# Kernel optimization log

Hardware: AMD Instinct MI355X
Metric: run time of the kernel (lower is better)

## Reference

```python
import jax, jax.numpy as jnp
import numpy as np

N = 10000
E = 160000
HEADS = 4
HC = 32      # hidden_channels
OC = 64      # out_channels
NG = 16      # n_goods
H1, H2 = 512, 256
NEG_SLOPE = 0.2


def setup_inputs() -> dict:
    key = jax.random.key(0)
    ks = jax.random.split(key, 32)
    rn = lambda k, s, sc=0.05: (jax.random.normal(k, s, jnp.float32) * sc)
    inp = {
        "x": jax.random.normal(ks[0], (N, 63), jnp.float32),
        "next_demand": jax.random.normal(ks[1], (N, 1), jnp.float32),
        "edge_index": jax.random.randint(ks[2], (2, E), 0, N),
        "eps": jax.random.normal(ks[3], (E, NG), jnp.float32),
        "Wl3": rn(ks[4], (HEADS * HC, 64)), "Wr3": rn(ks[5], (HEADS * HC, 64)),
        "att3": rn(ks[6], (HEADS, HC)), "b3": rn(ks[7], (HEADS * HC,)),
        # gat4: 128 -> 64, 1 head, mean
        "Wl4": rn(ks[8], (OC, HEADS * HC)), "Wr4": rn(ks[9], (OC, HEADS * HC)),
        "att4": rn(ks[10], (1, OC)), "b4": rn(ks[11], (OC,)),
        "Wl1": rn(ks[12], (HEADS * HC, OC)), "Wr1": rn(ks[13], (HEADS * HC, OC)),
        "att1": rn(ks[14], (HEADS, HC)), "b1": rn(ks[15], (HEADS * HC,)),
        # gat2: 128 -> 64, 1 head, mean
        "Wl2": rn(ks[16], (OC, HEADS * HC)), "Wr2": rn(ks[17], (OC, HEADS * HC)),
        "att2": rn(ks[18], (1, OC)), "b2": rn(ks[19], (OC,)),
        # MLP head: 256 -> 512 -> 256 -> n_goods (mu, std)
        "W_fc": rn(ks[20], (H1, OC * 4)), "b_fc": rn(ks[21], (H1,)),
        "W_fc1": rn(ks[22], (H2, H1)), "b_fc1": rn(ks[23], (H2,)),
        "W_mu": rn(ks[24], (NG, H2)), "b_mu": rn(ks[25], (NG,)),
        "W_std": rn(ks[26], (NG, H2)), "b_std": rn(ks[27], (NG,)),
    }
    return inp


def gatv2(x, src, dst, n, Wl, Wr, att, bias, heads, oc, concat):
    # GATv2Conv: e = a . LeakyReLU(Wl x_src + Wr x_dst), softmax over dst neighborhoods
    xl = (x @ Wl.T).reshape(n, heads, oc)
    xr = (x @ Wr.T).reshape(n, heads, oc)
    e = jax.nn.leaky_relu(xl[src] + xr[dst], NEG_SLOPE)        # [E', H, C]
    score = jnp.einsum('ehc,hc->eh', e, att)                   # [E', H]
    m = jax.ops.segment_max(score, dst, num_segments=n)        # stable segment softmax
    ex = jnp.exp(score - m[dst])
    den = jax.ops.segment_sum(ex, dst, num_segments=n)
    alpha = ex / (den[dst] + 1e-16)
    out = jax.ops.segment_sum(alpha[:, :, None] * xl[src], dst, num_segments=n)
    out = out.reshape(n, heads * oc) if concat else out.mean(axis=1)
    return out + bias


def reference(x, next_demand, edge_index, eps,
              Wl3, Wr3, att3, b3, Wl4, Wr4, att4, b4,
              Wl1, Wr1, att1, b1, Wl2, Wr2, att2, b2,
              W_fc, b_fc, W_fc1, b_fc1, W_mu, b_mu, W_std, b_std):
    n = x.shape[0]
    lrelu = lambda v: jax.nn.leaky_relu(v, NEG_SLOPE)
    loop = jnp.arange(n)
    # forward edges + self loops (PyG GATv2Conv add_self_loops=True)
    src = jnp.concatenate([edge_index[0], loop])
    dst = jnp.concatenate([edge_index[1], loop])
    # reverse edges + self loops
    rsrc = jnp.concatenate([edge_index[1], loop])
    rdst = jnp.concatenate([edge_index[0], loop])

    h = jnp.concatenate([x, next_demand.reshape(n, -1)], axis=1)   # [N, 64]
    xb = lrelu(gatv2(h, rsrc, rdst, n, Wl3, Wr3, att3, b3, HEADS, HC, True))
    xb = lrelu(gatv2(xb, rsrc, rdst, n, Wl4, Wr4, att4, b4, 1, OC, False))
    xf = lrelu(gatv2(xb, src, dst, n, Wl1, Wr1, att1, b1, HEADS, HC, True))
    xf = lrelu(gatv2(xf, src, dst, n, Wl2, Wr2, att2, b2, 1, OC, False))

    s = jnp.concatenate([xf, xb], axis=1)                          # [N, 128]
    se = jnp.concatenate([s[edge_index[0]], s[edge_index[1]]], axis=1)  # [E, 256]
    se = jax.nn.relu(se @ W_fc.T + b_fc)
    se = jax.nn.relu(se @ W_fc1.T + b_fc1)
    mu = se @ W_mu.T + b_mu
    std = jax.nn.softplus(se @ W_std.T + b_std)

    action = mu + std * eps                                        # rsample
    log2pi = jnp.log(2.0 * jnp.pi).astype(mu.dtype)
    lp = -0.5 * ((action - mu) / std) ** 2 - jnp.log(std) - 0.5 * log2pi
    log_prob = lp.reshape(1, -1).sum(-1, keepdims=True)            # num_graphs=1
    real_action = jnp.tanh(action)
    real_log_prob = log_prob - jnp.log(1.0 - real_action ** 2 + 1e-7).reshape(1, -1).sum(-1, keepdims=True)
    return (real_action.reshape(-1), real_log_prob)
```

## Files before the change

kernel.cpp:

```cpp
#include <hip/hip_runtime.h>
#include <hip/hip_bf16.h>
#include <math.h>

typedef __attribute__((ext_vector_type(8))) short short8;
typedef __attribute__((ext_vector_type(4))) float floatx4;

#define LRELU_S 0.2f
#define HALF_LOG_2PI 0.91893853320467274178f

__device__ __forceinline__ short f2bf(float f) {
  union { float f; unsigned u; } x; x.f = f;
  unsigned r = x.u + 0x7FFFu + ((x.u >> 16) & 1u);
  return (short)(r >> 16);
}
__device__ __forceinline__ float lrelu(float v) { return v > 0.f ? v : LRELU_S * v; }
__device__ __forceinline__ float frcp(float v) { return __builtin_amdgcn_rcpf(v); }
__device__ __forceinline__ float ftanh(float x) {
  float e = __expf(2.f * x);
  return 1.f - 2.f * frcp(e + 1.f);
}
__device__ __forceinline__ int swzb(int row) {
  return ((((row >> 2) & 3) << 1) | (row & 1)) << 4;
}

__global__ __launch_bounds__(256) void k_pre(const int* __restrict__ ei,
    int* __restrict__ degF, int* __restrict__ degR, int E,
    const float* __restrict__ x, const float* __restrict__ nd,
    float* __restrict__ h, int NH,
    const float* __restrict__ Wfc, const float* __restrict__ Wfc1,
    const float* __restrict__ Wmu, const float* __restrict__ Wstd,
    short* __restrict__ WBF, int nbE, int nbH) {
  int b = blockIdx.x;
  if (b < nbE) {
    int e = b * 256 + threadIdx.x;
    if (e < E) {
      int a = ei[e], bb = ei[E + e];
      atomicAdd(degF + bb, 1);
      atomicAdd(degR + a, 1);
    }
  } else if (b < nbE + nbH) {
    int t = (b - nbE) * 256 + threadIdx.x;
    if (t < NH) {
      int n = t >> 6, j = t & 63;
      h[t] = (j < 63) ? x[n * 63 + j] : nd[n];
    }
  } else {
    int t = (b - nbE - nbH) * 256 + threadIdx.x;
    if (t < 270336) {
      int tile = t >> 9, pos = t & 511;
      int lane = pos >> 3, j = pos & 7;
      int lr = lane & 15, lg = lane >> 4;
      float v;
      if (tile < 256) {
        int nt = tile >> 3, kk = tile & 7;
        v = Wfc[(nt * 16 + lr) * 256 + kk * 32 + lg * 8 + j];
      } else if (tile < 512) {
        int t2 = tile - 256;
        int nt = t2 >> 4, kk = t2 & 15;
        v = Wfc1[(nt * 16 + lr) * 512 + kk * 32 + lg * 8 + j];
      } else {
        int t3 = tile - 512;
        int nt = t3 >> 3, kk = t3 & 7;
        int r = nt * 16 + lr;
        int col = kk * 32 + lg * 8 + j;
        v = (r < 16) ? Wmu[r * 256 + col] : Wstd[(r - 16) * 256 + col];
      }
      WBF[t] = f2bf(v);
    }
  }
}

__global__ __launch_bounds__(1024) void k_scan2(const int* __restrict__ degF,
    int* __restrict__ startF, int* __restrict__ curF, int* __restrict__ csrF,
    const int* __restrict__ degR, int* __restrict__ startR, int* __restrict__ curR,
    int* __restrict__ csrR, int n) {
  const int* __restrict__ deg = blockIdx.x ? degR : degF;
  int* __restrict__ start = blockIdx.x ? startR : startF;
  int* __restrict__ cur   = blockIdx.x ? curR : curF;
  int* __restrict__ csr   = blockIdx.x ? csrR : csrF;
  __shared__ int wsum[16];
  int t = threadIdx.x;
  int chunk = (n + 1023) >> 10;
  int lo = t * chunk; if (lo > n) lo = n;
  int hi = lo + chunk; if (hi > n) hi = n;
  int s = 0;
  for (int i = lo; i < hi; i++) s += deg[i] + 1;
  int lane = t & 63, wv = t >> 6;
  int inc = s;
  #pragma unroll
  for (int o = 1; o < 64; o <<= 1) {
    int v = __shfl_up(inc, o, 64);
    if (lane >= o) inc += v;
  }
  if (lane == 63) wsum[wv] = inc;
  __syncthreads();
  if (t < 64) {
    int v = (t < 16) ? wsum[t] : 0;
    #pragma unroll
    for (int o = 1; o < 16; o <<= 1) {
      int u = __shfl_up(v, o, 64);
      if (t >= o) v += u;
    }
    if (t < 16) wsum[t] = v;
  }
  __syncthreads();
  int base = (wv ? wsum[wv - 1] : 0) + (inc - s);
  if (t == 0) start[n] = wsum[15];
  int acc = base;
  for (int i = lo; i < hi; i++) {
    start[i] = acc; cur[i] = acc;
    acc += deg[i] + 1;
    csr[acc - 1] = i;
  }
}

__global__ __launch_bounds__(256) void k_scatter(const int* __restrict__ ei,
    int* __restrict__ curF, int* __restrict__ curR,
    int* __restrict__ csrF, int* __restrict__ csrR, int E) {
  int e = blockIdx.x * 256 + threadIdx.x;
  if (e >= E) return;
  int a = ei[e], b = ei[E + e];
  int pf = atomicAdd(curF + b, 1); csrF[pf] = a;
  int pr = atomicAdd(curR + a, 1); csrR[pr] = b;
}

template<int K, int F>
__global__ __launch_bounds__(256) void k_node_gemm(const float* __restrict__ in,
    const float* __restrict__ Wl, const float* __restrict__ Wr,
    float* __restrict__ xl, float* __restrict__ xr, int n) {
  __shared__ float sx[32][K + 1];
  const int row0 = blockIdx.x * 32;
  const float* __restrict__ W = blockIdx.y ? Wr : Wl;
  float* __restrict__ out = blockIdx.y ? xr : xl;
  const int tid = threadIdx.x;
  for (int i = tid; i < 32 * K; i += 256) {
    int r = i / K, c = i - r * K;
    sx[r][c] = (row0 + r < n) ? in[(size_t)(row0 + r) * K + c] : 0.f;
  }
  __syncthreads();
  const int nl = tid & 31;
  const int fg = tid >> 5;
  const int row = row0 + nl;
  if (row >= n) return;
  constexpr int FP = F / 8;
  for (int i = 0; i < FP; i++) {
    int f = fg * FP + i;
    const float* __restrict__ wrow = W + (size_t)f * K;
    float acc = 0.f;
    #pragma unroll
    for (int k = 0; k < K; k += 4) {
      float4 wv = *(const float4*)(wrow + k);
      acc += sx[nl][k] * wv.x + sx[nl][k + 1] * wv.y
           + sx[nl][k + 2] * wv.z + sx[nl][k + 3] * wv.w;
    }
    out[(size_t)row * F + f] = acc;
  }
}

template<int HF, int C, int OM>
__global__ __launch_bounds__(256) void k_gat_fused(const float* __restrict__ XL,
    const float* __restrict__ XR, const float* __restrict__ att,
    const float* __restrict__ bias, const int* __restrict__ start,
    const int* __restrict__ csr, float* __restrict__ out,
    short* __restrict__ sout, int scol, int n) {
  constexpr int G = HF / 4;
  constexpr int DPB = 256 / G;
  int d = blockIdx.x * DPB + threadIdx.x / G;
  if (d >= n) return;
  int f4 = threadIdx.x & (G - 1);
  float4 xr = *(const float4*)(XR + (size_t)d * HF + f4 * 4);
  float4 av = *(const float4*)(att + f4 * 4);
  float4 bv = *(const float4*)(bias + f4 * 4);
  float m = -INFINITY, den = 0.f;
  float4 acc = {0.f, 0.f, 0.f, 0.f};
  int j0 = start[d], j1 = start[d + 1];

  auto score = [&](const float4& xl) {
    float e0 = xl.x + xr.x; e0 = e0 > 0.f ? e0 : LRELU_S * e0;
    float e1 = xl.y + xr.y; e1 = e1 > 0.f ? e1 : LRELU_S * e1;
    float e2 = xl.z + xr.z; e2 = e2 > 0.f ? e2 : LRELU_S * e2;
    float e3 = xl.w + xr.w; e3 = e3 > 0.f ? e3 : LRELU_S * e3;
    float p = av.x * e0 + av.y * e1 + av.z * e2 + av.w * e3;
    #pragma unroll
    for (int o = C / 8; o > 0; o >>= 1) p += __shfl_xor(p, o, 64);
    return p;
  };

  int j = j0;
  for (; j + 1 < j1; j += 2) {
    int sa = csr[j], sb = csr[j + 1];
    float4 xla = *(const float4*)(XL + (size_t)sa * HF + f4 * 4);
    float4 xlb = *(const float4*)(XL + (size_t)sb * HF + f4 * 4);
    float sca = score(xla);
    float scb = score(xlb);
    float mn = fmaxf(fmaxf(m, sca), scb);
    float scale = __expf(m - mn);
    float pa = __expf(sca - mn);
    float pb = __expf(scb - mn);
    den = den * scale + pa + pb;
    acc.x = acc.x * scale + pa * xla.x + pb * xlb.x;
    acc.y = acc.y * scale + pa * xla.y + pb * xlb.y;
    acc.z = acc.z * scale + pa * xla.z + pb * xlb.z;
    acc.w = acc.w * scale + pa * xla.w + pb * xlb.w;
    m = mn;
  }
  if (j < j1) {
    int s = csr[j];
    float4 xl = *(const float4*)(XL + (size_t)s * HF + f4 * 4);
    float sc = score(xl);
    float mn = fmaxf(m, sc);
    float scale = __expf(m - mn);
    float p = __expf(sc - mn);
    den = den * scale + p;
    acc.x = acc.x * scale + p * xl.x;
    acc.y = acc.y * scale + p * xl.y;
    acc.z = acc.z * scale + p * xl.z;
    acc.w = acc.w * scale + p * xl.w;
    m = mn;
  }
  float inv = frcp(den + 1e-16f);
  float4 o4;
  o4.x = lrelu(acc.x * inv + bv.x);
  o4.y = lrelu(acc.y * inv + bv.y);
  o4.z = lrelu(acc.z * inv + bv.z);
  o4.w = lrelu(acc.w * inv + bv.w);
  if (OM != 2) *(float4*)(out + (size_t)d * HF + f4 * 4) = o4;
  if (OM != 0) {
    union { short s[4]; int2 v; } u;
    u.s[0] = f2bf(o4.x); u.s[1] = f2bf(o4.y);
    u.s[2] = f2bf(o4.z); u.s[3] = f2bf(o4.w);
    *(int2*)(sout + (size_t)d * 128 + scol + f4 * 4) = u.v;
  }
}

__device__ __forceinline__ short8 lds_frag(const char* base, int row, int strideB, int k0, int lg) {
  int off = row * strideB + (((k0 * 2) + lg * 16) ^ swzb(row));
  return *(const short8*)(base + off);
}

__global__ __launch_bounds__(512, 4) void k_head(
    const short* __restrict__ SBF, const short* __restrict__ WBF,
    const int* __restrict__ ei, const float* __restrict__ epsg,
    const float* __restrict__ b_fc, const float* __restrict__ b_fc1,
    const float* __restrict__ b_mu, const float* __restrict__ b_std,
    float* __restrict__ out, double* __restrict__ LP, int E) {
  __shared__ __align__(16) char lX[32768];
  __shared__ __align__(16) char cbuf[16384];
  float* lMS  = (float*)cbuf;
  float* lred = (float*)(cbuf + 8192);

  const int tid = threadIdx.x;
  const int eg0 = blockIdx.x * 64;

  for (int q = tid; q < 2048; q += 512) {
    int le = q >> 5, c = q & 31;
    int eg = eg0 + le;
    int node = (c < 16) ? ei[eg] : ei[E + eg];
    const short* srcp = SBF + (size_t)node * 128 + (c & 15) * 8;
    int4 v = *(const int4*)srcp;
    int col = (c * 16) ^ swzb(le);
    *(int4*)(lX + le * 512 + col) = v;
  }
  __syncthreads();

  const int w = tid >> 6, lane = tid & 63;
  const int lr = lane & 15, lg = lane >> 4;
  const floatx4 zero = {0.f, 0.f, 0.f, 0.f};

  floatx4 acc2[2][4];
  #pragma unroll
  for (int a = 0; a < 2; a++)
    #pragma unroll
    for (int b = 0; b < 4; b++) acc2[a][b] = zero;

  for (int c = 0; c < 4; c++) {
    floatx4 acc1[4];
    #pragma unroll
    for (int mi = 0; mi < 4; mi++) acc1[mi] = zero;
    for (int kk = 0; kk < 8; kk++) {
      int tile = (c * 8 + w) * 8 + kk;
      short8 b = *(const short8*)(WBF + tile * 512 + lane * 8);
      #pragma unroll
      for (int mi = 0; mi < 4; mi++) {
        short8 a = lds_frag(lX, mi * 16 + lr, 512, kk * 32, lg);
        acc1[mi] = __builtin_amdgcn_mfma_f32_16x16x32_bf16(a, b, acc1[mi], 0, 0, 0);
      }
    }
    __syncthreads();
    {
      int cl = w * 16 + lr;
      float bv = b_fc[c * 128 + cl];
      #pragma unroll
      for (int mi = 0; mi < 4; mi++)
        #pragma unroll
        for (int j = 0; j < 4; j++) {
          int row = mi * 16 + lg * 4 + j;
          float v = acc1[mi][j] + bv;
          v = v > 0.f ? v : 0.f;
          *(short*)(cbuf + row * 256 + ((cl * 2) ^ swzb(row))) = f2bf(v);
        }
    }
    __syncthreads();

    for (int kk2 = 0; kk2 < 4; kk2++) {
      short8 a[4];
      #pragma unroll
      for (int mi = 0; mi < 4; mi++) a[mi] = lds_frag(cbuf, mi * 16 + lr, 256, kk2 * 32, lg);
      #pragma unroll
      for (int ni2 = 0; ni2 < 2; ni2++) {
        int tile = 256 + (2 * w + ni2) * 16 + (c * 4 + kk2);
        short8 b = *(const short8*)(WBF + tile * 512 + lane * 8);
        #pragma unroll
        for (int mi = 0; mi < 4; mi++)
          acc2[ni2][mi] = __builtin_amdgcn_mfma_f32_16x16x32_bf16(a[mi], b, acc2[ni2][mi], 0, 0, 0);
      }
    }
  }
  __syncthreads();

  #pragma unroll
  for (int ni2 = 0; ni2 < 2; ni2++) {
    int n = (2 * w + ni2) * 16 + lr;
    float bv = b_fc1[n];
    #pragma unroll
    for (int mi = 0; mi < 4; mi++)
      #pragma unroll
      for (int j = 0; j < 4; j++) {
        int row = mi * 16 + lg * 4 + j;
        float v = acc2[ni2][mi][j] + bv;
        v = v > 0.f ? v : 0.f;
        *(short*)(lX + row * 512 + ((n * 2) ^ swzb(row))) = f2bf(v);
      }
  }
  __syncthreads();

  {
    const int mfr = w >> 1, nfr = w & 1;
    floatx4 acc3 = zero;
    for (int kk = 0; kk < 8; kk++) {
      short8 a = lds_frag(lX, mfr * 16 + lr, 512, kk * 32, lg);
      int tile = 512 + nfr * 8 + kk;
      short8 b = *(const short8*)(WBF + tile * 512 + lane * 8);
      acc3 = __builtin_amdgcn_mfma_f32_16x16x32_bf16(a, b, acc3, 0, 0, 0);
    }
    int coln = nfr * 16 + lr;
    float bv = (coln < 16) ? b_mu[coln] : b_std[coln - 16];
    #pragma unroll
    for (int j = 0; j < 4; j++) {
      int row = mfr * 16 + lg * 4 + j;
      lMS[row * 32 + coln] = acc3[j] + bv;
    }
  }
  __syncthreads();

  float lpsum = 0.f;
  #pragma unroll
  for (int it = 0; it < 2; it++) {
    int idx = tid + it * 512;
    int m = idx >> 4, g = idx & 15;
    float mu = lMS[m * 32 + g];
    float sr = lMS[m * 32 + 16 + g];
    float sd = (sr > 20.f) ? sr : __logf(1.f + __expf(sr));
    int eg = eg0 + m;
    float ep = epsg[(size_t)eg * 16 + g];
    float action = mu + sd * ep;
    float ra = ftanh(action);
    out[(size_t)eg * 16 + g] = ra;
    lpsum += -0.5f * ep * ep - __logf(sd) - HALF_LOG_2PI - __logf(1.f - ra * ra + 1e-7f);
  }
  #pragma unroll
  for (int o = 32; o > 0; o >>= 1) lpsum += __shfl_xor(lpsum, o, 64);
  if (lane == 0) lred[w] = lpsum;
  __syncthreads();
  if (tid == 0) {
    double ssum = 0.0;
    #pragma unroll
    for (int i = 0; i < 8; i++) ssum += (double)lred[i];
    atomicAdd(LP, ssum);
  }
}

__global__ void k_finalize(const double* __restrict__ LP, float* __restrict__ out, int pos) {
  out[pos] = (float)(*LP);
}

extern "C" void kernel_launch(void* const* d_in, const int* in_sizes, int n_in,
                              void* d_out, int out_size, void* d_ws, size_t ws_size,
                              hipStream_t stream) {
  const float* x    = (const float*)d_in[0];
  const float* nd   = (const float*)d_in[1];
  const int*   ei   = (const int*)d_in[2];
  const float* epsg = (const float*)d_in[3];
  const float* Wl3 = (const float*)d_in[4];  const float* Wr3 = (const float*)d_in[5];
  const float* att3 = (const float*)d_in[6]; const float* b3 = (const float*)d_in[7];
  const float* Wl4 = (const float*)d_in[8];  const float* Wr4 = (const float*)d_in[9];
  const float* att4 = (const float*)d_in[10]; const float* b4 = (const float*)d_in[11];
  const float* Wl1 = (const float*)d_in[12]; const float* Wr1 = (const float*)d_in[13];
  const float* att1 = (const float*)d_in[14]; const float* b1 = (const float*)d_in[15];
  const float* Wl2 = (const float*)d_in[16]; const float* Wr2 = (const float*)d_in[17];
  const float* att2 = (const float*)d_in[18]; const float* b2 = (const float*)d_in[19];
  const float* W_fc  = (const float*)d_in[20]; const float* b_fc  = (const float*)d_in[21];
  const float* W_fc1 = (const float*)d_in[22]; const float* b_fc1 = (const float*)d_in[23];
  const float* W_mu  = (const float*)d_in[24]; const float* b_mu  = (const float*)d_in[25];
  const float* W_std = (const float*)d_in[26]; const float* b_std = (const float*)d_in[27];

  const int N = in_sizes[0] / 63;
  const int E = in_sizes[2] / 2;
  const int E2 = E + N;
  const size_t NN = (size_t)N;

  char* base = (char*)d_ws;
  auto alloc = [&](size_t bytes) { char* p = base; base += (bytes + 15) & ~(size_t)15; return p; };

  int* degF   = (int*)alloc(NN * 4);
  int* degR   = (int*)alloc(NN * 4);
  double* LPp = (double*)alloc(16);
  float* bufA = (float*)alloc(NN * 128 * 4);
  float* bufB = (float*)alloc(NN * 128 * 4);
  float* XL   = (float*)alloc(NN * 128 * 4);
  float* XR   = (float*)alloc(NN * 128 * 4);
  float* XBp  = (float*)alloc(NN * 64 * 4);
  int* curF   = (int*)alloc(NN * 4);
  int* curR   = (int*)alloc(NN * 4);
  int* startF = (int*)alloc((NN + 1) * 4);
  int* startR = (int*)alloc((NN + 1) * 4);
  int* csrF   = (int*)alloc((size_t)E2 * 4);
  int* csrR   = (int*)alloc((size_t)E2 * 4);
  short* SBF  = (short*)alloc(NN * 128 * 2);
  short* WBF  = (short*)alloc(270336 * 2);

  auto nb = [](int total) { return (total + 255) / 256; };
  const int nbE = nb(E), nbH = nb(N * 64), nbW = nb(270336);

  hipMemsetAsync(degF, 0, NN * 8 + 16, stream);

  k_pre<<<nbE + nbH + nbW, 256, 0, stream>>>(ei, degF, degR, E, x, nd, bufA, N * 64,
                                             W_fc, W_fc1, W_mu, W_std, WBF, nbE, nbH);
  k_scan2<<<2, 1024, 0, stream>>>(degF, startF, curF, csrF, degR, startR, curR, csrR, N);
  k_scatter<<<nbE, 256, 0, stream>>>(ei, curF, curR, csrF, csrR, E);

  { dim3 g((N + 31) / 32, 2);
    k_node_gemm<64, 128><<<g, 256, 0, stream>>>(bufA, Wl3, Wr3, XL, XR, N); }
  k_gat_fused<128, 32, 0><<<(N + 7) / 8, 256, 0, stream>>>(XL, XR, att3, b3, startR, csrR, bufB, nullptr, 0, N);

  { dim3 g((N + 31) / 32, 2);
    k_node_gemm<128, 64><<<g, 256, 0, stream>>>(bufB, Wl4, Wr4, XL, XR, N); }
  k_gat_fused<64, 64, 1><<<(N + 15) / 16, 256, 0, stream>>>(XL, XR, att4, b4, startR, csrR, XBp, SBF, 64, N);

  { dim3 g((N + 31) / 32, 2);
    k_node_gemm<64, 128><<<g, 256, 0, stream>>>(XBp, Wl1, Wr1, XL, XR, N); }
  k_gat_fused<128, 32, 0><<<(N + 7) / 8, 256, 0, stream>>>(XL, XR, att1, b1, startF, csrF, bufB, nullptr, 0, N);

  { dim3 g((N + 31) / 32, 2);
    k_node_gemm<128, 64><<<g, 256, 0, stream>>>(bufB, Wl2, Wr2, XL, XR, N); }
  k_gat_fused<64, 64, 2><<<(N + 15) / 16, 256, 0, stream>>>(XL, XR, att2, b2, startF, csrF, nullptr, SBF, 0, N);

  k_head<<<E / 64, 512, 0, stream>>>(SBF, WBF, ei, epsg, b_fc, b_fc1, b_mu, b_std,
                                     (float*)d_out, LPp, E);
  k_finalize<<<1, 1, 0, stream>>>(LPp, (float*)d_out, E * 16);
}
```

Baseline: 434.1 us.

## Fuse next-layer node projection into GAT aggregation kernels and concat into first GEMM

Each GAT aggregation kernel now keeps its per-node output in shared memory and immediately computes the next layer's left/right projections, writing them into ping-pong XL/XR buffers. This drops three separate node-GEMM launches and the round trip of intermediate activations through global memory. The x/next_demand concatenation moves from k_pre into the first node GEMM's load loop. In exchange, each aggregation block now does a small GEMM that rereads the weight rows per output and adds a block barrier, which may lower occupancy and lengthen each aggregation kernel.

```diff
diff --git a/kernel.cpp b/kernel.cpp
--- a/kernel.cpp
+++ b/kernel.cpp
@@ -25,11 +25,9 @@
 
 __global__ __launch_bounds__(256) void k_pre(const int* __restrict__ ei,
     int* __restrict__ degF, int* __restrict__ degR, int E,
-    const float* __restrict__ x, const float* __restrict__ nd,
-    float* __restrict__ h, int NH,
     const float* __restrict__ Wfc, const float* __restrict__ Wfc1,
     const float* __restrict__ Wmu, const float* __restrict__ Wstd,
-    short* __restrict__ WBF, int nbE, int nbH) {
+    short* __restrict__ WBF, int nbE) {
   int b = blockIdx.x;
   if (b < nbE) {
     int e = b * 256 + threadIdx.x;
@@ -38,14 +36,8 @@
       atomicAdd(degF + bb, 1);
       atomicAdd(degR + a, 1);
     }
-  } else if (b < nbE + nbH) {
+  } else {
     int t = (b - nbE) * 256 + threadIdx.x;
-    if (t < NH) {
-      int n = t >> 6, j = t & 63;
-      h[t] = (j < 63) ? x[n * 63 + j] : nd[n];
-    }
-  } else {
-    int t = (b - nbE - nbH) * 256 + threadIdx.x;
     if (t < 270336) {
       int tile = t >> 9, pos = t & 511;
       int lane = pos >> 3, j = pos & 7;
@@ -124,18 +116,21 @@
   int pr = atomicAdd(curR + a, 1); csrR[pr] = b;
 }
 
-template<int K, int F>
-__global__ __launch_bounds__(256) void k_node_gemm(const float* __restrict__ in,
-    const float* __restrict__ Wl, const float* __restrict__ Wr,
-    float* __restrict__ xl, float* __restrict__ xr, int n) {
+__global__ __launch_bounds__(256) void k_node_gemm0(const float* __restrict__ x,
+    const float* __restrict__ nd, const float* __restrict__ Wl,
+    const float* __restrict__ Wr, float* __restrict__ xl, float* __restrict__ xr, int n) {
+  constexpr int K = 64, F = 128;
   __shared__ float sx[32][K + 1];
   const int row0 = blockIdx.x * 32;
   const float* __restrict__ W = blockIdx.y ? Wr : Wl;
   float* __restrict__ out = blockIdx.y ? xr : xl;
   const int tid = threadIdx.x;
   for (int i = tid; i < 32 * K; i += 256) {
-    int r = i / K, c = i - r * K;
-    sx[r][c] = (row0 + r < n) ? in[(size_t)(row0 + r) * K + c] : 0.f;
+    int r = i >> 6, c = i & 63;
+    int row = row0 + r;
+    float v = 0.f;
+    if (row < n) v = (c < 63) ? x[row * 63 + c] : nd[row];
+    sx[r][c] = v;
   }
   __syncthreads();
   const int nl = tid & 31;
@@ -157,79 +152,109 @@
   }
 }
 
-template<int HF, int C, int OM>
-__global__ __launch_bounds__(256) void k_gat_fused(const float* __restrict__ XL,
+template<int HF, int C, int OUTK, int OM>
+__global__ __launch_bounds__(256) void k_gat_gemm(const float* __restrict__ XL,
     const float* __restrict__ XR, const float* __restrict__ att,
     const float* __restrict__ bias, const int* __restrict__ start,
-    const int* __restrict__ csr, float* __restrict__ out,
+    const int* __restrict__ csr,
+    const float* __restrict__ Wl, const float* __restrict__ Wr,
+    float* __restrict__ oXL, float* __restrict__ oXR,
     short* __restrict__ sout, int scol, int n) {
   constexpr int G = HF / 4;
   constexpr int DPB = 256 / G;
-  int d = blockIdx.x * DPB + threadIdx.x / G;
-  if (d >= n) return;
-  int f4 = threadIdx.x & (G - 1);
-  float4 xr = *(const float4*)(XR + (size_t)d * HF + f4 * 4);
-  float4 av = *(const float4*)(att + f4 * 4);
-  float4 bv = *(const float4*)(bias + f4 * 4);
-  float m = -INFINITY, den = 0.f;
-  float4 acc = {0.f, 0.f, 0.f, 0.f};
-  int j0 = start[d], j1 = start[d + 1];
-
-  auto score = [&](const float4& xl) {
-    float e0 = xl.x + xr.x; e0 = e0 > 0.f ? e0 : LRELU_S * e0;
-    float e1 = xl.y + xr.y; e1 = e1 > 0.f ? e1 : LRELU_S * e1;
-    float e2 = xl.z + xr.z; e2 = e2 > 0.f ? e2 : LRELU_S * e2;
-    float e3 = xl.w + xr.w; e3 = e3 > 0.f ? e3 : LRELU_S * e3;
-    float p = av.x * e0 + av.y * e1 + av.z * e2 + av.w * e3;
-    #pragma unroll
-    for (int o = C / 8; o > 0; o >>= 1) p += __shfl_xor(p, o, 64);
-    return p;
-  };
-
-  int j = j0;
-  for (; j + 1 < j1; j += 2) {
-    int sa = csr[j], sb = csr[j + 1];
-    float4 xla = *(const float4*)(XL + (size_t)sa * HF + f4 * 4);
-    float4 xlb = *(const float4*)(XL + (size_t)sb * HF + f4 * 4);
-    float sca = score(xla);
-    float scb = score(xlb);
-    float mn = fmaxf(fmaxf(m, sca), scb);
-    float scale = __expf(m - mn);
-    float pa = __expf(sca - mn);
-    float pb = __expf(scb - mn);
-    den = den * scale + pa + pb;
-    acc.x = acc.x * scale + pa * xla.x + pb * xlb.x;
-    acc.y = acc.y * scale + pa * xla.y + pb * xlb.y;
-    acc.z = acc.z * scale + pa * xla.z + pb * xlb.z;
-    acc.w = acc.w * scale + pa * xla.w + pb * xlb.w;
-    m = mn;
-  }
-  if (j < j1) {
-    int s = csr[j];
-    float4 xl = *(const float4*)(XL + (size_t)s * HF + f4 * 4);
-    float sc = score(xl);
-    float mn = fmaxf(m, sc);
-    float scale = __expf(m - mn);
-    float p = __expf(sc - mn);
-    den = den * scale + p;
-    acc.x = acc.x * scale + p * xl.x;
-    acc.y = acc.y * scale + p * xl.y;
-    acc.z = acc.z * scale + p * xl.z;
-    acc.w = acc.w * scale + p * xl.w;
-    m = mn;
-  }
-  float inv = frcp(den + 1e-16f);
-  float4 o4;
-  o4.x = lrelu(acc.x * inv + bv.x);
-  o4.y = lrelu(acc.y * inv + bv.y);
-  o4.z = lrelu(acc.z * inv + bv.z);
-  o4.w = lrelu(acc.w * inv + bv.w);
-  if (OM != 2) *(float4*)(out + (size_t)d * HF + f4 * 4) = o4;
-  if (OM != 0) {
-    union { short s[4]; int2 v; } u;
-    u.s[0] = f2bf(o4.x); u.s[1] = f2bf(o4.y);
-    u.s[2] = f2bf(o4.z); u.s[3] = f2bf(o4.w);
-    *(int2*)(sout + (size_t)d * 128 + scol + f4 * 4) = u.v;
+  __shared__ float sg[DPB][HF];
+  const int tid = threadIdx.x;
+  const int grp = tid / G;
+  const int d = blockIdx.x * DPB + grp;
+  const int f4 = tid & (G - 1);
+
+  if (d < n) {
+    float4 xr = *(const float4*)(XR + (size_t)d * HF + f4 * 4);
+    float4 av = *(const float4*)(att + f4 * 4);
+    float4 bv = *(const float4*)(bias + f4 * 4);
+    float m = -INFINITY, den = 0.f;
+    float4 acc = {0.f, 0.f, 0.f, 0.f};
+    int j0 = start[d], j1 = start[d + 1];
+
+    auto score = [&](const float4& xl) {
+      float e0 = xl.x + xr.x; e0 = e0 > 0.f ? e0 : LRELU_S * e0;
+      float e1 = xl.y + xr.y; e1 = e1 > 0.f ? e1 : LRELU_S * e1;
+      float e2 = xl.z + xr.z; e2 = e2 > 0.f ? e2 : LRELU_S * e2;
+      float e3 = xl.w + xr.w; e3 = e3 > 0.f ? e3 : LRELU_S * e3;
+      float p = av.x * e0 + av.y * e1 + av.z * e2 + av.w * e3;
+      #pragma unroll
+      for (int o = C / 8; o > 0; o >>= 1) p += __shfl_xor(p, o, 64);
+      return p;
+    };
+
+    int j = j0;
+    for (; j + 1 < j1; j += 2) {
+      int sa = csr[j], sb = csr[j + 1];
+      float4 xla = *(const float4*)(XL + (size_t)sa * HF + f4 * 4);
+      float4 xlb = *(const float4*)(XL + (size_t)sb * HF + f4 * 4);
+      float sca = score(xla);
+      float scb = score(xlb);
+      float mn = fmaxf(fmaxf(m, sca), scb);
+      float scale = __expf(m - mn);
+      float pa = __expf(sca - mn);
+      float pb = __expf(scb - mn);
+      den = den * scale + pa + pb;
+      acc.x = acc.x * scale + pa * xla.x + pb * xlb.x;
+      acc.y = acc.y * scale + pa * xla.y + pb * xlb.y;
+      acc.z = acc.z * scale + pa * xla.z + pb * xlb.z;
+      acc.w = acc.w * scale + pa * xla.w + pb * xlb.w;
+      m = mn;
+    }
+    if (j < j1) {
+      int s = csr[j];
+      float4 xl = *(const float4*)(XL + (size_t)s * HF + f4 * 4);
+      float sc = score(xl);
+      float mn = fmaxf(m, sc);
+      float scale = __expf(m - mn);
+      float p = __expf(sc - mn);
+      den = den * scale + p;
+      acc.x = acc.x * scale + p * xl.x;
+      acc.y = acc.y * scale + p * xl.y;
+      acc.z = acc.z * scale + p * xl.z;
+      acc.w = acc.w * scale + p * xl.w;
+      m = mn;
+    }
+    float inv = frcp(den + 1e-16f);
+    float4 o4;
+    o4.x = lrelu(acc.x * inv + bv.x);
+    o4.y = lrelu(acc.y * inv + bv.y);
+    o4.z = lrelu(acc.z * inv + bv.z);
+    o4.w = lrelu(acc.w * inv + bv.w);
+    if (OM) {
+      union { short s[4]; int2 v; } u;
+      u.s[0] = f2bf(o4.x); u.s[1] = f2bf(o4.y);
+      u.s[2] = f2bf(o4.z); u.s[3] = f2bf(o4.w);
+      *(int2*)(sout + (size_t)d * 128 + scol + f4 * 4) = u.v;
+    }
+    *(float4*)(&sg[grp][f4 * 4]) = o4;
+  }
+
+  if constexpr (OUTK > 0) {
+    __syncthreads();
+    constexpr int TOT = DPB * 2 * OUTK;
+    for (int i = 0; i < TOT / 256; i++) {
+      int idx = tid + i * 256;
+      int r = idx / (2 * OUTK), c = idx % (2 * OUTK);
+      int drow = blockIdx.x * DPB + r;
+      if (drow < n) {
+        const float* __restrict__ wrow =
+            (c < OUTK) ? (Wl + (size_t)c * HF) : (Wr + (size_t)(c - OUTK) * HF);
+        float acc = 0.f;
+        #pragma unroll
+        for (int k = 0; k < HF; k += 4) {
+          float4 wv = *(const float4*)(wrow + k);
+          float4 sv = *(const float4*)(&sg[r][k]);
+          acc += sv.x * wv.x + sv.y * wv.y + sv.z * wv.z + sv.w * wv.w;
+        }
+        if (c < OUTK) oXL[(size_t)drow * OUTK + c] = acc;
+        else          oXR[(size_t)drow * OUTK + (c - OUTK)] = acc;
+      }
+    }
   }
 }
 
@@ -415,11 +440,10 @@
   int* degF   = (int*)alloc(NN * 4);
   int* degR   = (int*)alloc(NN * 4);
   double* LPp = (double*)alloc(16);
-  float* bufA = (float*)alloc(NN * 128 * 4);
-  float* bufB = (float*)alloc(NN * 128 * 4);
-  float* XL   = (float*)alloc(NN * 128 * 4);
-  float* XR   = (float*)alloc(NN * 128 * 4);
-  float* XBp  = (float*)alloc(NN * 64 * 4);
+  float* XLa  = (float*)alloc(NN * 128 * 4);
+  float* XRa  = (float*)alloc(NN * 128 * 4);
+  float* XLb  = (float*)alloc(NN * 128 * 4);
+  float* XRb  = (float*)alloc(NN * 128 * 4);
   int* curF   = (int*)alloc(NN * 4);
   int* curR   = (int*)alloc(NN * 4);
   int* startF = (int*)alloc((NN + 1) * 4);
@@ -430,30 +454,28 @@
   short* WBF  = (short*)alloc(270336 * 2);
 
   auto nb = [](int total) { return (total + 255) / 256; };
-  const int nbE = nb(E), nbH = nb(N * 64), nbW = nb(270336);
+  const int nbE = nb(E), nbW = nb(270336);
 
   hipMemsetAsync(degF, 0, NN * 8 + 16, stream);
 
-  k_pre<<<nbE + nbH + nbW, 256, 0, stream>>>(ei, degF, degR, E, x, nd, bufA, N * 64,
-                                             W_fc, W_fc1, W_mu, W_std, WBF, nbE, nbH);
+  k_pre<<<nbE + nbW, 256, 0, stream>>>(ei, degF, degR, E, W_fc, W_fc1, W_mu, W_std, WBF, nbE);
   k_scan2<<<2, 1024, 0, stream>>>(degF, startF, curF, csrF, degR, startR, curR, csrR, N);
   k_scatter<<<nbE, 256, 0, stream>>>(ei, curF, curR, csrF, csrR, E);
 
   { dim3 g((N + 31) / 32, 2);
-    k_node_gemm<64, 128><<<g, 256, 0, stream>>>(bufA, Wl3, Wr3, XL, XR, N); }
-  k_gat_fused<128, 32, 0><<<(N + 7) / 8, 256, 0, stream>>>(XL, XR, att3, b3, startR, csrR, bufB, nullptr, 0, N);
-
-  { dim3 g((N + 31) / 32, 2);
-    k_node_gemm<128, 64><<<g, 256, 0, stream>>>(bufB, Wl4, Wr4, XL, XR, N); }
-  k_gat_fused<64, 64, 1><<<(N + 15) / 16, 256, 0, stream>>>(XL, XR, att4, b4, startR, csrR, XBp, SBF, 64, N);
-
-  { dim3 g((N + 31) / 32, 2);
-    k_node_gemm<64, 128><<<g, 256, 0, stream>>>(XBp, Wl1, Wr1, XL, XR, N); }
-  k_gat_fused<128, 32, 0><<<(N + 7) / 8, 256, 0, stream>>>(XL, XR, att1, b1, startF, csrF, bufB, nullptr, 0, N);
-
-  { dim3 g((N + 31) / 32, 2);
-    k_node_gemm<128, 64><<<g, 256, 0, stream>>>(bufB, Wl2, Wr2, XL, XR, N); }
-  k_gat_fused<64, 64, 2><<<(N + 15) / 16, 256, 0, stream>>>(XL, XR, att2, b2, startF, csrF, nullptr, SBF, 0, N);
+    k_node_gemm0<<<g, 256, 0, stream>>>(x, nd, Wl3, Wr3, XLa, XRa, N); }
+
+  k_gat_gemm<128, 32, 64, 0><<<(N + 7) / 8, 256, 0, stream>>>(
+      XLa, XRa, att3, b3, startR, csrR, Wl4, Wr4, XLb, XRb, nullptr, 0, N);
+
+  k_gat_gemm<64, 64, 128, 1><<<(N + 15) / 16, 256, 0, stream>>>(
+      XLb, XRb, att4, b4, startR, csrR, Wl1, Wr1, XLa, XRa, SBF, 64, N);
+
+  k_gat_gemm<128, 32, 64, 0><<<(N + 7) / 8, 256, 0, stream>>>(
+      XLa, XRa, att1, b1, startF, csrF, Wl2, Wr2, XLb, XRb, nullptr, 0, N);
+
+  k_gat_gemm<64, 64, 0, 1><<<(N + 15) / 16, 256, 0, stream>>>(
+      XLb, XRb, att2, b2, startF, csrF, nullptr, nullptr, nullptr, nullptr, SBF, 0, N);
 
   k_head<<<E / 64, 512, 0, stream>>>(SBF, WBF, ei, epsg, b_fc, b_fc1, b_mu, b_std,
                                      (float*)d_out, LPp, E);
```

Result: slower. 509.2 us (+17.3%).
